# Kernel tuning notes

Hardware: AMD Instinct MI355X
Metric: run time of the kernel (lower is better)

The kernel has to match this reference:

```python
import jax, jax.numpy as jnp
import numpy as np

S, L, IN_DIM, PROJ, OUT = 128, 512, 256, 32, 128


def _layernorm(x, eps=1e-5):
    mu = jnp.mean(x, axis=-1, keepdims=True)
    var = jnp.var(x, axis=-1, keepdims=True)
    return (x - mu) * jax.lax.rsqrt(var + eps)


def setup_inputs() -> dict:
    key = jax.random.key(0)
    k0, k1, k2 = jax.random.split(key, 3)
    return {
        "node_repr": jax.random.normal(k0, (S, L, IN_DIM), dtype=jnp.float32),
        "mask": jnp.ones((S, L), dtype=jnp.float32),
        # nn.Linear(in_dim, 2*proj_dim): weight [2*proj, in], bias [2*proj]
        "w_proj": jax.random.normal(k1, (2 * PROJ, IN_DIM), dtype=jnp.float32) * 0.02,
        "b_proj": jnp.zeros((2 * PROJ,), dtype=jnp.float32),
        "out_weights": jax.random.normal(k2, (PROJ, PROJ, OUT), dtype=jnp.float32) * 0.02,
        "out_bias": jnp.zeros((OUT,), dtype=jnp.float32),
    }


def reference(node_repr, mask, w_proj, b_proj, out_weights, out_bias):
    # normalize over channel dim (parameter-free layer norm, as utils.tnormalize)
    x = _layernorm(node_repr)                     # [s, i, in_dim]
    act = x @ w_proj.T + b_proj                   # [s, i, 2*proj]
    act = act * mask[..., None]
    l = act[..., :PROJ]                           # [s, i, d]
    r = act[..., PROJ:]                           # [s, j, e]
    # norm = einsum('sid,sjd->ijd', mask[...,None], mask[...,None]) -> [i, j, 1]
    norm = jnp.einsum('si,sj->ij', mask, mask)[..., None]
    # outer-product-mean: contract MSA dim s, then mix (d,e) -> f
    out = jnp.einsum('sid,def,sje->ijf', l, out_weights, r, optimize=True)
    out = out + out_bias
    return out / (norm + 0.001)
```

## Files before the change

kernel.cpp:

```cpp
#include <hip/hip_runtime.h>
#include <cstdint>

#define S_DIM 128
#define L_DIM 512
#define INimD 256
#define OUTF  128

typedef __bf16 bf16x8 __attribute__((ext_vector_type(8)));
typedef float  f32x16 __attribute__((ext_vector_type(16)));

__device__ __forceinline__ unsigned short f2bf(float f) {
  unsigned int u = __float_as_uint(f);
  u = (u + 0x7fffu + ((u >> 16) & 1u)) >> 16;
  return (unsigned short)u;
}

__global__ __launch_bounds__(256) void k_wp(const float* __restrict__ w,
                                            unsigned short* __restrict__ WP)
{
  const int gid = blockIdx.x * 256 + threadIdx.x;
  const int ln = gid & 63, t = gid >> 6;
  const int nt = t & 1, kt = t >> 1;
  const int j  = nt * 32 + (ln & 31);
  const int k0 = kt * 16 + (ln >> 5) * 8;
#pragma unroll
  for (int jj = 0; jj < 8; ++jj)
    WP[(size_t)gid * 8 + jj] = f2bf(w[(size_t)j * INimD + k0 + jj]);
}

__global__ __launch_bounds__(256) void k_lnproj(
    const float* __restrict__ x, const float* __restrict__ mask,
    const unsigned short* __restrict__ WP, const float* __restrict__ b,
    unsigned short* __restrict__ l_t, unsigned short* __restrict__ r_t)
{
  __shared__ unsigned short smem[128 * 256];
  __shared__ float msk[128];
  const int tid = threadIdx.x;
  const int wv = tid >> 6, lane = tid & 63;
  const int half = lane >> 5, ln = lane & 31;
  const int l = blockIdx.x;

  if (tid < 128) msk[tid] = mask[(size_t)tid * L_DIM + l];

  for (int bi = 0; bi < 8; ++bi) {
    const int r0 = wv * 32 + bi * 4;
    float4 v[4];
#pragma unroll
    for (int q = 0; q < 4; ++q)
      v[q] = ((const float4*)(x + ((size_t)(r0 + q) * L_DIM + l) * INimD))[lane];
#pragma unroll
    for (int q = 0; q < 4; ++q) {
      float sm = v[q].x + v[q].y + v[q].z + v[q].w;
      float sq = v[q].x*v[q].x + v[q].y*v[q].y + v[q].z*v[q].z + v[q].w*v[q].w;
#pragma unroll
      for (int off = 32; off > 0; off >>= 1) {
        sm += __shfl_xor(sm, off);
        sq += __shfl_xor(sq, off);
      }
      const float mu  = sm * (1.0f / 256.0f);
      const float var = sq * (1.0f / 256.0f) - mu * mu;
      const float rs  = rsqrtf(var + 1e-5f);
      const int r = r0 + q;
      ushort4 hp;
      hp.x = f2bf((v[q].x - mu) * rs);
      hp.y = f2bf((v[q].y - mu) * rs);
      hp.z = f2bf((v[q].z - mu) * rs);
      hp.w = f2bf((v[q].w - mu) * rs);
      const int col = (lane * 4) ^ ((r & 7) << 3);
      *(ushort4*)&smem[r * 256 + col] = hp;
    }
  }
  __syncthreads();

  f32x16 acc0, acc1;
#pragma unroll
  for (int q = 0; q < 16; ++q) { acc0[q] = 0.f; acc1[q] = 0.f; }
  const int ar = wv * 32 + ln;
#pragma unroll
  for (int kt = 0; kt < 16; ++kt) {
    const int col = (kt * 16 + half * 8) ^ ((ln & 7) << 3);
    bf16x8 a  = *(const bf16x8*)&smem[ar * 256 + col];
    bf16x8 b0 = *(const bf16x8*)(WP + ((size_t)((kt * 2 + 0) * 64 + lane)) * 8);
    bf16x8 b1 = *(const bf16x8*)(WP + ((size_t)((kt * 2 + 1) * 64 + lane)) * 8);
    acc0 = __builtin_amdgcn_mfma_f32_32x32x16_bf16(a, b0, acc0, 0, 0, 0);
    acc1 = __builtin_amdgcn_mfma_f32_32x32x16_bf16(a, b1, acc1, 0, 0, 0);
  }
  __syncthreads();

  unsigned short (*act)[136] = (unsigned short(*)[136])smem;
  const float bj0 = b[ln];
  const float bj1 = b[32 + ln];
#pragma unroll
  for (int nt = 0; nt < 2; ++nt) {
    const f32x16 a = nt ? acc1 : acc0;
    const float bj = nt ? bj1 : bj0;
    const int j = nt * 32 + ln;
#pragma unroll
    for (int g = 0; g < 4; ++g) {
      const int s0 = wv * 32 + g * 8 + half * 4;
      ushort4 p;
      p.x = f2bf((a[g*4+0] + bj) * msk[s0+0]);
      p.y = f2bf((a[g*4+1] + bj) * msk[s0+1]);
      p.z = f2bf((a[g*4+2] + bj) * msk[s0+2]);
      p.w = f2bf((a[g*4+3] + bj) * msk[s0+3]);
      *(ushort4*)&act[j][s0] = p;
    }
  }
  __syncthreads();

  const int d = tid >> 2, c = (tid & 3) * 32;
  uint4 outv[4];
  ushort4* pv = (ushort4*)outv;
#pragma unroll
  for (int q = 0; q < 8; ++q) pv[q] = *(ushort4*)&act[d][c + q * 4];
  unsigned short* dst = (d < 32)
      ? (l_t + ((size_t)l * 32 + d) * S_DIM + c)
      : (r_t + ((size_t)l * 32 + (d - 32)) * S_DIM + c);
  ((uint4*)dst)[0] = outv[0];
  ((uint4*)dst)[1] = outv[1];
  ((uint4*)dst)[2] = outv[2];
  ((uint4*)dst)[3] = outv[3];
}

__global__ __launch_bounds__(256) void k_norm(const float* __restrict__ mask,
                                              float* __restrict__ recip)
{
  const int i = blockIdx.y * 16 + (threadIdx.x >> 4);
  const int j = blockIdx.x * 16 + (threadIdx.x & 15);
  float acc = 0.f;
  for (int s = 0; s < S_DIM; ++s)
    acc += mask[(size_t)s * L_DIM + i] * mask[(size_t)s * L_DIM + j];
  recip[(size_t)i * L_DIM + j] = 1.0f / (acc + 0.001f);
}

__global__ __launch_bounds__(256) void k_wb(const float* __restrict__ W,
                                            unsigned short* __restrict__ WB)
{
  const int gid = blockIdx.x * 256 + threadIdx.x;
  const int ln = gid & 63;
  const int ftkt = gid >> 6;
  const int ft = ftkt & 3, kt = ftkt >> 2;
  const int f  = ft * 32 + (ln & 31);
  const int kb = kt * 16 + (ln >> 5) * 8;
#pragma unroll
  for (int jj = 0; jj < 8; ++jj) {
    const int k = kb + jj;
    WB[(size_t)gid * 8 + jj] = f2bf(W[(size_t)k * OUTF + f]);
  }
}

__global__ __launch_bounds__(256, 2) void k_pair(
    const unsigned short* __restrict__ l_t, const unsigned short* __restrict__ r_t,
    const unsigned short* __restrict__ WB, const float* __restrict__ recip,
    const float* __restrict__ bias, float* __restrict__ out)
{
  __shared__ __align__(16) unsigned short r_lds[128][136];
  __shared__ __align__(16) unsigned short l_lds[32][136];
  __shared__ __align__(16) unsigned short g_lds[64][72];
  const int tid = threadIdx.x;
  const int wv = tid >> 6, lane = tid & 63;
  const int half = lane >> 5, ln = lane & 31;
  const int j0 = blockIdx.x * 4, i0 = blockIdx.y * 16;

  {
    const int row = tid >> 1, off = (tid & 1) * 64;
    const uint4* src = (const uint4*)(r_t + ((size_t)j0 * 32 + row) * S_DIM + off);
    uint4* dst = (uint4*)&r_lds[row][off];
#pragma unroll
    for (int q = 0; q < 8; ++q) dst[q] = src[q];
  }

  f32x16 acc0, acc1;
#pragma unroll
  for (int q = 0; q < 16; ++q) { acc0[q] = 0.f; acc1[q] = 0.f; }

  for (int c = 0; c < 16; ++c) {
    {
      const int row = tid >> 3, off = (tid & 7) * 16;
      const int ii = row & 15, dc = row >> 4;
      const uint4* src = (const uint4*)(l_t + (((size_t)(i0 + ii)) * 32 + 2 * c + dc) * S_DIM + off);
      uint4* dst = (uint4*)&l_lds[row][off];
      dst[0] = src[0]; dst[1] = src[1];
    }
    __syncthreads();

    f32x16 g;
#pragma unroll
    for (int q = 0; q < 16; ++q) g[q] = 0.f;
#pragma unroll
    for (int s8 = 0; s8 < 8; ++s8) {
      const int soff = s8 * 16 + half * 8;
      bf16x8 a  = *(const bf16x8*)&l_lds[ln][soff];
      bf16x8 bb = *(const bf16x8*)&r_lds[wv * 32 + ln][soff];
      g = __builtin_amdgcn_mfma_f32_32x32x16_bf16(a, bb, g, 0, 0, 0);
    }
    __syncthreads();
#pragma unroll
    for (int reg = 0; reg < 16; ++reg) {
      const int r  = (reg & 3) + 8 * (reg >> 2) + 4 * half;
      const int p  = (r & 15) * 4 + wv;
      const int kl = (r >> 4) * 32 + ln;
      g_lds[p][kl] = f2bf(g[reg]);
    }
    __syncthreads();

#pragma unroll
    for (int kt = 0; kt < 4; ++kt) {
      const int gkt = c * 4 + kt;
      bf16x8 bw = *(const bf16x8*)(WB + ((size_t)(gkt * 4 + wv) * 64 + lane) * 8);
      bf16x8 a0 = *(const bf16x8*)&g_lds[ln][kt * 16 + half * 8];
      bf16x8 a1 = *(const bf16x8*)&g_lds[32 + ln][kt * 16 + half * 8];
      acc0 = __builtin_amdgcn_mfma_f32_32x32x16_bf16(a0, bw, acc0, 0, 0, 0);
      acc1 = __builtin_amdgcn_mfma_f32_32x32x16_bf16(a1, bw, acc1, 0, 0, 0);
    }
  }

  const float bi = bias[wv * 32 + ln];
#pragma unroll
  for (int mt = 0; mt < 2; ++mt) {
    const f32x16 a = mt ? acc1 : acc0;
#pragma unroll
    for (int reg = 0; reg < 16; ++reg) {
      const int p = mt * 32 + (reg & 3) + 8 * (reg >> 2) + 4 * half;
      const int i = i0 + (p >> 2), j = j0 + (p & 3);
      const float val = (a[reg] + bi) * recip[(size_t)i * L_DIM + j];
      out[((size_t)i * L_DIM + j) * OUTF + wv * 32 + ln] = val;
    }
  }
}

extern "C" void kernel_launch(void* const* d_in, const int* in_sizes, int n_in,
                              void* d_out, int out_size, void* d_ws, size_t ws_size,
                              hipStream_t stream) {
  const float* x    = (const float*)d_in[0];
  const float* mask = (const float*)d_in[1];
  const float* w    = (const float*)d_in[2];
  const float* b    = (const float*)d_in[3];
  const float* W    = (const float*)d_in[4];
  const float* bias = (const float*)d_in[5];
  float* out = (float*)d_out;

  char* ws = (char*)d_ws;
  unsigned short* l_t = (unsigned short*)ws;
  unsigned short* r_t = (unsigned short*)(ws + (4u << 20));
  unsigned short* WB  = (unsigned short*)(ws + (8u << 20));
  float* recip = (float*)(ws + (8u << 20) + (512u << 10));
  unsigned short* WP  = (unsigned short*)(ws + (8u << 20) + (512u << 10) + (1u << 20));

  hipLaunchKernelGGL(k_wp,     dim3(8),        dim3(256), 0, stream, w, WP);
  hipLaunchKernelGGL(k_lnproj, dim3(512),      dim3(256), 0, stream, x, mask, WP, b, l_t, r_t);
  hipLaunchKernelGGL(k_norm,   dim3(32, 32),   dim3(256), 0, stream, mask, recip);
  hipLaunchKernelGGL(k_wb,     dim3(64),       dim3(256), 0, stream, W, WB);
  hipLaunchKernelGGL(k_pair,   dim3(128, 32),  dim3(256), 0, stream, l_t, r_t, WB, recip, bias, out);
}
```

Measured before the change: 350.8 us.

## Double-buffer pair kernel LDS with async global-to-LDS loads and register-held r tiles

The pair kernel now keeps each wave's r tile in registers instead of LDS. It streams l tiles into a double-buffered, XOR-swizzled LDS region with global_load_lds, and double-buffers the g staging buffer so each chunk needs one barrier instead of three. It also prefetches WB weights ahead of the MFMAs and raises the occupancy hint to 3 blocks per CU. The norm kernel now stages the mask columns in shared memory. The aim is to overlap loads with MFMA work and cut synchronisation, at the cost of more register pressure and tighter ordering between the async LDS loads and the barriers.

```diff
diff --git a/kernel.cpp b/kernel.cpp
--- a/kernel.cpp
+++ b/kernel.cpp
@@ -7,12 +7,19 @@
 #define OUTF  128
 
 typedef __bf16 bf16x8 __attribute__((ext_vector_type(8)));
+typedef __bf16 bf16x4 __attribute__((ext_vector_type(4)));
 typedef float  f32x16 __attribute__((ext_vector_type(16)));
 
 __device__ __forceinline__ unsigned short f2bf(float f) {
   unsigned int u = __float_as_uint(f);
   u = (u + 0x7fffu + ((u >> 16) & 1u)) >> 16;
   return (unsigned short)u;
+}
+
+__device__ __forceinline__ void gload_lds16(const void* gsrc, void* ldst) {
+  __builtin_amdgcn_global_load_lds(
+      (const __attribute__((address_space(1))) unsigned int*)gsrc,
+      (__attribute__((address_space(3))) unsigned int*)ldst, 16, 0, 0);
 }
 
 __global__ __launch_bounds__(256) void k_wp(const float* __restrict__ w,
@@ -125,12 +132,20 @@
 __global__ __launch_bounds__(256) void k_norm(const float* __restrict__ mask,
                                               float* __restrict__ recip)
 {
-  const int i = blockIdx.y * 16 + (threadIdx.x >> 4);
-  const int j = blockIdx.x * 16 + (threadIdx.x & 15);
+  __shared__ float mi[128][16];
+  __shared__ float mj[128][16];
+  const int i0 = blockIdx.y * 16, j0 = blockIdx.x * 16;
+  for (int idx = threadIdx.x; idx < 2048; idx += 256) {
+    const int s = idx >> 4, cc = idx & 15;
+    mi[s][cc] = mask[(size_t)s * L_DIM + i0 + cc];
+    mj[s][cc] = mask[(size_t)s * L_DIM + j0 + cc];
+  }
+  __syncthreads();
+  const int ti = threadIdx.x >> 4, tj = threadIdx.x & 15;
   float acc = 0.f;
-  for (int s = 0; s < S_DIM; ++s)
-    acc += mask[(size_t)s * L_DIM + i] * mask[(size_t)s * L_DIM + j];
-  recip[(size_t)i * L_DIM + j] = 1.0f / (acc + 0.001f);
+#pragma unroll 8
+  for (int s = 0; s < 128; ++s) acc += mi[s][ti] * mj[s][tj];
+  recip[(size_t)(i0 + ti) * L_DIM + j0 + tj] = 1.0f / (acc + 0.001f);
 }
 
 __global__ __launch_bounds__(256) void k_wb(const float* __restrict__ W,
@@ -149,69 +164,90 @@
   }
 }
 
-__global__ __launch_bounds__(256, 2) void k_pair(
+__global__ __launch_bounds__(256, 3) void k_pair(
     const unsigned short* __restrict__ l_t, const unsigned short* __restrict__ r_t,
     const unsigned short* __restrict__ WB, const float* __restrict__ recip,
     const float* __restrict__ bias, float* __restrict__ out)
 {
-  __shared__ __align__(16) unsigned short r_lds[128][136];
-  __shared__ __align__(16) unsigned short l_lds[32][136];
-  __shared__ __align__(16) unsigned short g_lds[64][72];
+  __shared__ __align__(16) unsigned short l_lds[2][32][128];
+  __shared__ __align__(16) unsigned short g_lds[2][64][68];
   const int tid = threadIdx.x;
   const int wv = tid >> 6, lane = tid & 63;
   const int half = lane >> 5, ln = lane & 31;
   const int j0 = blockIdx.x * 4, i0 = blockIdx.y * 16;
 
-  {
-    const int row = tid >> 1, off = (tid & 1) * 64;
-    const uint4* src = (const uint4*)(r_t + ((size_t)j0 * 32 + row) * S_DIM + off);
-    uint4* dst = (uint4*)&r_lds[row][off];
-#pragma unroll
-    for (int q = 0; q < 8; ++q) dst[q] = src[q];
-  }
+  bf16x8 rf[8];
+#pragma unroll
+  for (int s8 = 0; s8 < 8; ++s8)
+    rf[s8] = *(const bf16x8*)(r_t + ((size_t)(j0 + wv) * 32 + ln) * S_DIM
+                                  + s8 * 16 + half * 8);
+
+  const unsigned short* lsrc[2];
+#pragma unroll
+  for (int t = 0; t < 2; ++t) {
+    const int r_ = wv * 8 + t * 4 + (lane >> 4);
+    const int gg = lane & 15;
+    lsrc[t] = l_t + ((size_t)(i0 + (r_ & 15)) * 32 + (r_ >> 4)) * S_DIM
+                  + ((gg ^ (r_ & 7)) * 8);
+  }
+#pragma unroll
+  for (int t = 0; t < 2; ++t)
+    gload_lds16(lsrc[t], &l_lds[0][wv * 8 + t * 4][0]);
 
   f32x16 acc0, acc1;
 #pragma unroll
   for (int q = 0; q < 16; ++q) { acc0[q] = 0.f; acc1[q] = 0.f; }
 
+  const int pr  = (ln & 15) * 4 + wv;
+  const int dcc = ln >> 4;
+
+  __syncthreads();
+
   for (int c = 0; c < 16; ++c) {
+    const int cur = c & 1;
+    if (c < 15) {
+#pragma unroll
+      for (int t = 0; t < 2; ++t) {
+        lsrc[t] += 256;
+        gload_lds16(lsrc[t], &l_lds[cur ^ 1][wv * 8 + t * 4][0]);
+      }
+    }
+    bf16x8 bw[4];
+#pragma unroll
+    for (int kt = 0; kt < 4; ++kt)
+      bw[kt] = *(const bf16x8*)(WB + ((size_t)((c * 4 + kt) * 4 + wv) * 64 + lane) * 8);
+
+    f32x16 g;
+#pragma unroll
+    for (int q = 0; q < 16; ++q) g[q] = 0.f;
+#pragma unroll
+    for (int s8 = 0; s8 < 8; ++s8) {
+      const int col = ((s8 * 2 + half) ^ (ln & 7)) * 8;
+      bf16x8 bl = *(const bf16x8*)&l_lds[cur][ln][col];
+      g = __builtin_amdgcn_mfma_f32_32x32x16_bf16(rf[s8], bl, g, 0, 0, 0);
+    }
     {
-      const int row = tid >> 3, off = (tid & 7) * 16;
-      const int ii = row & 15, dc = row >> 4;
-      const uint4* src = (const uint4*)(l_t + (((size_t)(i0 + ii)) * 32 + 2 * c + dc) * S_DIM + off);
-      uint4* dst = (uint4*)&l_lds[row][off];
-      dst[0] = src[0]; dst[1] = src[1];
+      unsigned short* gp = &g_lds[cur][pr][dcc * 32 + 4 * half];
+#pragma unroll
+      for (int q = 0; q < 4; ++q) {
+        ushort4 hp;
+        hp.x = f2bf(g[4*q+0]); hp.y = f2bf(g[4*q+1]);
+        hp.z = f2bf(g[4*q+2]); hp.w = f2bf(g[4*q+3]);
+        *(ushort4*)(gp + q * 8) = hp;
+      }
     }
     __syncthreads();
 
-    f32x16 g;
-#pragma unroll
-    for (int q = 0; q < 16; ++q) g[q] = 0.f;
-#pragma unroll
-    for (int s8 = 0; s8 < 8; ++s8) {
-      const int soff = s8 * 16 + half * 8;
-      bf16x8 a  = *(const bf16x8*)&l_lds[ln][soff];
-      bf16x8 bb = *(const bf16x8*)&r_lds[wv * 32 + ln][soff];
-      g = __builtin_amdgcn_mfma_f32_32x32x16_bf16(a, bb, g, 0, 0, 0);
-    }
-    __syncthreads();
-#pragma unroll
-    for (int reg = 0; reg < 16; ++reg) {
-      const int r  = (reg & 3) + 8 * (reg >> 2) + 4 * half;
-      const int p  = (r & 15) * 4 + wv;
-      const int kl = (r >> 4) * 32 + ln;
-      g_lds[p][kl] = f2bf(g[reg]);
-    }
-    __syncthreads();
-
 #pragma unroll
     for (int kt = 0; kt < 4; ++kt) {
-      const int gkt = c * 4 + kt;
-      bf16x8 bw = *(const bf16x8*)(WB + ((size_t)(gkt * 4 + wv) * 64 + lane) * 8);
-      bf16x8 a0 = *(const bf16x8*)&g_lds[ln][kt * 16 + half * 8];
-      bf16x8 a1 = *(const bf16x8*)&g_lds[32 + ln][kt * 16 + half * 8];
-      acc0 = __builtin_amdgcn_mfma_f32_32x32x16_bf16(a0, bw, acc0, 0, 0, 0);
-      acc1 = __builtin_amdgcn_mfma_f32_32x32x16_bf16(a1, bw, acc1, 0, 0, 0);
+      const unsigned short* p0 = &g_lds[cur][ln][kt * 16 + half * 8];
+      const unsigned short* p1 = &g_lds[cur][32 + ln][kt * 16 + half * 8];
+      bf16x4 a0l = *(const bf16x4*)p0, a0h = *(const bf16x4*)(p0 + 4);
+      bf16x4 a1l = *(const bf16x4*)p1, a1h = *(const bf16x4*)(p1 + 4);
+      bf16x8 a0 = __builtin_shufflevector(a0l, a0h, 0,1,2,3,4,5,6,7);
+      bf16x8 a1 = __builtin_shufflevector(a1l, a1h, 0,1,2,3,4,5,6,7);
+      acc0 = __builtin_amdgcn_mfma_f32_32x32x16_bf16(a0, bw[kt], acc0, 0, 0, 0);
+      acc1 = __builtin_amdgcn_mfma_f32_32x32x16_bf16(a1, bw[kt], acc1, 0, 0, 0);
     }
   }
 
```

Result: faster. 337.4 us (-3.8%).
